# Performance work log

Hardware: AMD Instinct MI355X
Metric: run time of the kernel (lower is better)

## Reference

```python
import jax, jax.numpy as jnp
import numpy as np

B, D_IN, UNITS = 8192, 4096, 4096

def setup_inputs() -> dict:
    key = jax.random.key(0)
    k1, k2 = jax.random.split(key)
    x = jax.random.normal(k1, (B, D_IN), dtype=jnp.float32)
    kernel = jax.random.normal(k2, (D_IN, UNITS), dtype=jnp.float32) * 0.02  # glorot-ish scale
    bias = jnp.zeros((UNITS,), dtype=jnp.float32)
    return {"x": x, "kernel": kernel, "bias": bias}

def reference(x, kernel, bias):
    # BinaryDense: binarize weights via sign, then dense matmul + bias
    kernel_bin = jnp.sign(kernel)                     # [D_IN, UNITS], values in {-1,0,+1}
    out = jnp.matmul(x, kernel_bin) + bias            # [B, UNITS]
    return out
```

## Files before the change

### kernel.cpp

```cpp
#include <hip/hip_runtime.h>
#include <stdint.h>


typedef int int4v __attribute__((ext_vector_type(4)));

constexpr int M = 8192, N = 4096, K = 4096;
constexpr int BM = 256, BN = 256, BK = 128;
constexpr int NT = K / BK;
constexpr int NIT = NT / 2;

__device__ __forceinline__ void gload_lds16(const void* g, void* l) {
  __builtin_amdgcn_global_load_lds(
      (const __attribute__((address_space(1))) unsigned int*)g,
      (__attribute__((address_space(3))) unsigned int*)l, 16, 0, 0);
}

__global__ __launch_bounds__(256) void quant_x_kernel(const float* __restrict__ x,
                                                      signed char* __restrict__ xq,
                                                      float* __restrict__ rscale) {
  const int row = blockIdx.x;
  const int t = threadIdx.x;
  const float* xr = x + (size_t)row * K;
  float4 v[4];
  float mx = 0.f;
#pragma unroll
  for (int i = 0; i < 4; ++i) {
    v[i] = *(const float4*)(xr + t * 16 + i * 4);
    mx = fmaxf(mx, fmaxf(fmaxf(fabsf(v[i].x), fabsf(v[i].y)),
                         fmaxf(fabsf(v[i].z), fabsf(v[i].w))));
  }
#pragma unroll
  for (int off = 32; off >= 1; off >>= 1)
    mx = fmaxf(mx, __shfl_xor(mx, off, 64));
  __shared__ float smax[4];
  if ((t & 63) == 0) smax[t >> 6] = mx;
  __syncthreads();
  const float rm = fmaxf(fmaxf(smax[0], smax[1]), fmaxf(smax[2], smax[3]));
  const float s = (rm > 0.f) ? 127.f / rm : 0.f;
  if (t == 0) rscale[row] = (rm > 0.f) ? rm / 127.f : 0.f;
  uint32_t o[4];
#pragma unroll
  for (int i = 0; i < 4; ++i) {
    float f[4] = {v[i].x, v[i].y, v[i].z, v[i].w};
    uint32_t p = 0;
#pragma unroll
    for (int j = 0; j < 4; ++j) {
      int q = (int)rintf(f[j] * s);
      p |= ((uint32_t)(uint8_t)(signed char)q) << (8 * j);
    }
    o[i] = p;
  }
  *(int4v*)(xq + (size_t)row * K + t * 16) = (int4v){(int)o[0], (int)o[1], (int)o[2], (int)o[3]};
}

__global__ __launch_bounds__(256) void sign_t_kernel(const float* __restrict__ w,
                                                     signed char* __restrict__ wq) {
  __shared__ __align__(16) signed char tile[64 * 68];
  const int n0 = blockIdx.x * 64, k0 = blockIdx.y * 64;
  const int t = threadIdx.x;
#pragma unroll
  for (int i = 0; i < 4; ++i) {
    int kl = (t >> 4) + i * 16;
    int nl = (t & 15) * 4;
    float4 v = *(const float4*)(w + (size_t)(k0 + kl) * N + n0 + nl);
    uint32_t p = 0;
    p |= ((uint32_t)(uint8_t)(signed char)((v.x > 0.f) - (v.x < 0.f)));
    p |= ((uint32_t)(uint8_t)(signed char)((v.y > 0.f) - (v.y < 0.f))) << 8;
    p |= ((uint32_t)(uint8_t)(signed char)((v.z > 0.f) - (v.z < 0.f))) << 16;
    p |= ((uint32_t)(uint8_t)(signed char)((v.w > 0.f) - (v.w < 0.f))) << 24;
    *(uint32_t*)(tile + kl * 68 + nl) = p;
  }
  __syncthreads();
  const int nl = t >> 2;
  const int kc = (t & 3) * 16;
  uint32_t o[4] = {0, 0, 0, 0};
#pragma unroll
  for (int j = 0; j < 16; ++j)
    o[j >> 2] |= ((uint32_t)(uint8_t)tile[(kc + j) * 68 + nl]) << (8 * (j & 3));
  *(int4v*)(wq + (size_t)(n0 + nl) * K + k0 + kc) =
      (int4v){(int)o[0], (int)o[1], (int)o[2], (int)o[3]};
}


#define PHASE(BUF, MIH, NIH, LOADB, ...)                                         \
  {                                                                              \
    asm volatile("s_waitcnt vmcnt(6)" ::: "memory");                             \
    int4v a_[4][2];                                                              \
    _Pragma("unroll") for (int mi_ = 0; mi_ < 4; ++mi_) {                        \
      _Pragma("unroll") for (int kk_ = 0; kk_ < 2; ++kk_) {                      \
        const int row_ = wm * 128 + ((MIH)*4 + mi_) * 16 + l16;                  \
        const int c_ = kk_ * 4 + quad;                                           \
        a_[mi_][kk_] = *(const int4v*)(smem + (BUF)*65536 + row_ * 128 +         \
                                       ((c_ ^ (row_ & 7)) * 16));                \
      }                                                                          \
    }                                                                            \
    if (LOADB) {                                                                 \
      _Pragma("unroll") for (int nj_ = 0; nj_ < 2; ++nj_) {                      \
        _Pragma("unroll") for (int kk_ = 0; kk_ < 2; ++kk_) {                    \
          const int row_ = wn * 64 + ((NIH)*2 + nj_) * 16 + l16;                 \
          const int c_ = kk_ * 4 + quad;                                         \
          breg[nj_][kk_] = *(const int4v*)(smem + (BUF)*65536 + 32768 +          \
                                           row_ * 128 + ((c_ ^ (row_ & 7)) * 16)); \
        }                                                                        \
      }                                                                          \
    }                                                                            \
    __VA_ARGS__;                                                                 \
    __builtin_amdgcn_s_barrier();                                                \
    asm volatile("s_waitcnt lgkmcnt(0)" ::: "memory");                           \
    __builtin_amdgcn_s_setprio(1);                                               \
    _Pragma("unroll") for (int mi_ = 0; mi_ < 4; ++mi_) {                        \
      _Pragma("unroll") for (int nj_ = 0; nj_ < 2; ++nj_) {                      \
        _Pragma("unroll") for (int kk_ = 0; kk_ < 2; ++kk_) {                    \
          acc[(MIH)*4 + mi_][(NIH)*2 + nj_] =                                    \
              __builtin_amdgcn_mfma_i32_16x16x64_i8(                             \
                  a_[mi_][kk_], breg[nj_][kk_],                                  \
                  acc[(MIH)*4 + mi_][(NIH)*2 + nj_], 0, 0, 0);                   \
        }                                                                        \
      }                                                                          \
    }                                                                            \
    __builtin_amdgcn_s_setprio(0);                                               \
    __builtin_amdgcn_s_barrier();                                                \
  }

__global__ __launch_bounds__(512, 2) void gemm_bin_kernel(
    const signed char* __restrict__ Xq,
    const signed char* __restrict__ Wq,
    const float* __restrict__ rscale,
    const float* __restrict__ bias,
    float* __restrict__ out) {
  __shared__ __align__(16) signed char smem[131072];

  const int tid = threadIdx.x;
  const int w = tid >> 6;
  const int lane = tid & 63;
  const int wm = w >> 2;
  const int wn = w & 3;
  const int quad = lane >> 4;
  const int l16 = lane & 15;
  const size_t m0 = (size_t)blockIdx.y * BM;
  const size_t n0 = (size_t)blockIdx.x * BN;

  int4v acc[8][4];
#pragma unroll
  for (int i = 0; i < 8; ++i)
#pragma unroll
    for (int j = 0; j < 4; ++j) acc[i][j] = (int4v){0, 0, 0, 0};
  int4v breg[2][2];

  auto stageA = [&](int buf, int half, int tile) {
    signed char* lb = smem + buf * 65536;
#pragma unroll
    for (int it = 0; it < 2; ++it) {
      int pos = it * 512 + tid;
      int rr = pos >> 3, s = pos & 7;
      int row = half * 64 + (rr & 63) + (rr >> 6) * 128;
      int qg = s ^ (row & 7);
      gload_lds16(Xq + (m0 + row) * (size_t)K + (size_t)tile * BK + qg * 16,
                  lb + row * 128 + s * 16);
    }
  };
  auto stageB = [&](int buf, int half, int tile) {
    signed char* lb = smem + buf * 65536 + 32768;
#pragma unroll
    for (int it = 0; it < 2; ++it) {
      int pos = it * 512 + tid;
      int rr = pos >> 3, s = pos & 7;
      int row = half * 32 + (rr & 31) + (rr >> 5) * 64;
      int qg = s ^ (row & 7);
      gload_lds16(Wq + (n0 + row) * (size_t)K + (size_t)tile * BK + qg * 16,
                  lb + row * 128 + s * 16);
    }
  };

  stageB(0, 0, 0);
  stageA(0, 0, 0);
  stageA(0, 1, 0);
  stageB(0, 1, 0);
  stageB(1, 0, 1);
  stageA(1, 0, 1);
  asm volatile("s_waitcnt vmcnt(6)" ::: "memory");
  __builtin_amdgcn_s_barrier();

#pragma unroll 1
  for (int i = 0; i < NIT; ++i) {
    const int t1 = 2 * i + 1, t2 = 2 * i + 2, t3 = 2 * i + 3;
    const bool more = (i + 1 < NIT);
    PHASE(0, 0, 0, true,  { stageA(1, 1, t1); })
    PHASE(0, 1, 0, false, { stageB(1, 1, t1); })
    PHASE(0, 0, 1, true,  { if (more) stageB(0, 0, t2); })
    PHASE(0, 1, 1, false, { if (more) stageA(0, 0, t2); })
    PHASE(1, 0, 0, true,  { if (more) stageA(0, 1, t2); })
    PHASE(1, 1, 0, false, { if (more) stageB(0, 1, t2); })
    PHASE(1, 0, 1, true,  { if (more) stageB(1, 0, t3); })
    PHASE(1, 1, 1, false, { if (more) stageA(1, 0, t3); })
  }

#pragma unroll
  for (int mi = 0; mi < 8; ++mi) {
    const size_t rbase = m0 + wm * 128 + mi * 16 + quad * 4;
    float sc[4];
#pragma unroll
    for (int r = 0; r < 4; ++r) sc[r] = rscale[rbase + r];
#pragma unroll
    for (int ni = 0; ni < 4; ++ni) {
      const size_t col = n0 + wn * 64 + ni * 16 + l16;
      const float bv = bias[col];
#pragma unroll
      for (int r = 0; r < 4; ++r)
        out[(rbase + r) * N + col] = (float)acc[mi][ni][r] * sc[r] + bv;
    }
  }
}

extern "C" void kernel_launch(void* const* d_in, const int* in_sizes, int n_in,
                              void* d_out, int out_size, void* d_ws, size_t ws_size,
                              hipStream_t stream) {
  const float* x = (const float*)d_in[0];
  const float* kern = (const float*)d_in[1];
  const float* bias = (const float*)d_in[2];
  float* out = (float*)d_out;

  signed char* Xq = (signed char*)d_ws;
  signed char* Wq = Xq + (size_t)M * K;
  float* rscale = (float*)(Wq + (size_t)N * K);

  quant_x_kernel<<<M, 256, 0, stream>>>(x, Xq, rscale);
  sign_t_kernel<<<dim3(N / 64, K / 64), dim3(256), 0, stream>>>(kern, Wq);
  gemm_bin_kernel<<<dim3(N / BN, M / BM), 512, 0, stream>>>(Xq, Wq, rscale, bias, out);
}
```

Before: 394.6 us.

## Merge prep kernels and restructure GEMM pipeline to prefetch LDS fragments ahead of MFMA

Merges the x-quantization and weight sign-transpose kernels into one launch, removing one kernel launch and the serialization between them. The int8 GEMM main loop is reworked so each phase first issues the MFMAs on fragments already held in registers. It then reads the next phase's A/B fragments from LDS and issues the next global-to-LDS stage, with one barrier per phase instead of two. The tile staging order is reshuffled to match, and vmcnt is loosened to 4. This aims to overlap LDS reads with MFMA work, but adds register pressure from holding full A fragments and risks subtle LDS buffer hazards if the staging order is wrong.

```diff
diff --git a/kernel.cpp b/kernel.cpp
--- a/kernel.cpp
+++ b/kernel.cpp
@@ -15,111 +15,115 @@
       (__attribute__((address_space(3))) unsigned int*)l, 16, 0, 0);
 }
 
-__global__ __launch_bounds__(256) void quant_x_kernel(const float* __restrict__ x,
-                                                      signed char* __restrict__ xq,
-                                                      float* __restrict__ rscale) {
-  const int row = blockIdx.x;
+__global__ __launch_bounds__(256) void prep_kernel(const float* __restrict__ x,
+                                                   signed char* __restrict__ xq,
+                                                   float* __restrict__ rscale,
+                                                   const float* __restrict__ w,
+                                                   signed char* __restrict__ wq) {
   const int t = threadIdx.x;
-  const float* xr = x + (size_t)row * K;
-  float4 v[4];
-  float mx = 0.f;
-#pragma unroll
-  for (int i = 0; i < 4; ++i) {
-    v[i] = *(const float4*)(xr + t * 16 + i * 4);
-    mx = fmaxf(mx, fmaxf(fmaxf(fabsf(v[i].x), fabsf(v[i].y)),
-                         fmaxf(fabsf(v[i].z), fabsf(v[i].w))));
-  }
-#pragma unroll
-  for (int off = 32; off >= 1; off >>= 1)
-    mx = fmaxf(mx, __shfl_xor(mx, off, 64));
-  __shared__ float smax[4];
-  if ((t & 63) == 0) smax[t >> 6] = mx;
-  __syncthreads();
-  const float rm = fmaxf(fmaxf(smax[0], smax[1]), fmaxf(smax[2], smax[3]));
-  const float s = (rm > 0.f) ? 127.f / rm : 0.f;
-  if (t == 0) rscale[row] = (rm > 0.f) ? rm / 127.f : 0.f;
-  uint32_t o[4];
-#pragma unroll
-  for (int i = 0; i < 4; ++i) {
-    float f[4] = {v[i].x, v[i].y, v[i].z, v[i].w};
-    uint32_t p = 0;
-#pragma unroll
-    for (int j = 0; j < 4; ++j) {
-      int q = (int)rintf(f[j] * s);
-      p |= ((uint32_t)(uint8_t)(signed char)q) << (8 * j);
-    }
-    o[i] = p;
-  }
-  *(int4v*)(xq + (size_t)row * K + t * 16) = (int4v){(int)o[0], (int)o[1], (int)o[2], (int)o[3]};
-}
-
-__global__ __launch_bounds__(256) void sign_t_kernel(const float* __restrict__ w,
-                                                     signed char* __restrict__ wq) {
-  __shared__ __align__(16) signed char tile[64 * 68];
-  const int n0 = blockIdx.x * 64, k0 = blockIdx.y * 64;
-  const int t = threadIdx.x;
-#pragma unroll
-  for (int i = 0; i < 4; ++i) {
-    int kl = (t >> 4) + i * 16;
-    int nl = (t & 15) * 4;
-    float4 v = *(const float4*)(w + (size_t)(k0 + kl) * N + n0 + nl);
-    uint32_t p = 0;
-    p |= ((uint32_t)(uint8_t)(signed char)((v.x > 0.f) - (v.x < 0.f)));
-    p |= ((uint32_t)(uint8_t)(signed char)((v.y > 0.f) - (v.y < 0.f))) << 8;
-    p |= ((uint32_t)(uint8_t)(signed char)((v.z > 0.f) - (v.z < 0.f))) << 16;
-    p |= ((uint32_t)(uint8_t)(signed char)((v.w > 0.f) - (v.w < 0.f))) << 24;
-    *(uint32_t*)(tile + kl * 68 + nl) = p;
-  }
-  __syncthreads();
-  const int nl = t >> 2;
-  const int kc = (t & 3) * 16;
-  uint32_t o[4] = {0, 0, 0, 0};
-#pragma unroll
-  for (int j = 0; j < 16; ++j)
-    o[j >> 2] |= ((uint32_t)(uint8_t)tile[(kc + j) * 68 + nl]) << (8 * (j & 3));
-  *(int4v*)(wq + (size_t)(n0 + nl) * K + k0 + kc) =
-      (int4v){(int)o[0], (int)o[1], (int)o[2], (int)o[3]};
-}
-
-
-#define PHASE(BUF, MIH, NIH, LOADB, ...)                                         \
-  {                                                                              \
-    asm volatile("s_waitcnt vmcnt(6)" ::: "memory");                             \
-    int4v a_[4][2];                                                              \
-    _Pragma("unroll") for (int mi_ = 0; mi_ < 4; ++mi_) {                        \
-      _Pragma("unroll") for (int kk_ = 0; kk_ < 2; ++kk_) {                      \
-        const int row_ = wm * 128 + ((MIH)*4 + mi_) * 16 + l16;                  \
-        const int c_ = kk_ * 4 + quad;                                           \
-        a_[mi_][kk_] = *(const int4v*)(smem + (BUF)*65536 + row_ * 128 +         \
-                                       ((c_ ^ (row_ & 7)) * 16));                \
-      }                                                                          \
-    }                                                                            \
-    if (LOADB) {                                                                 \
-      _Pragma("unroll") for (int nj_ = 0; nj_ < 2; ++nj_) {                      \
-        _Pragma("unroll") for (int kk_ = 0; kk_ < 2; ++kk_) {                    \
-          const int row_ = wn * 64 + ((NIH)*2 + nj_) * 16 + l16;                 \
-          const int c_ = kk_ * 4 + quad;                                         \
-          breg[nj_][kk_] = *(const int4v*)(smem + (BUF)*65536 + 32768 +          \
-                                           row_ * 128 + ((c_ ^ (row_ & 7)) * 16)); \
-        }                                                                        \
-      }                                                                          \
-    }                                                                            \
-    __VA_ARGS__;                                                                 \
-    __builtin_amdgcn_s_barrier();                                                \
-    asm volatile("s_waitcnt lgkmcnt(0)" ::: "memory");                           \
-    __builtin_amdgcn_s_setprio(1);                                               \
-    _Pragma("unroll") for (int mi_ = 0; mi_ < 4; ++mi_) {                        \
-      _Pragma("unroll") for (int nj_ = 0; nj_ < 2; ++nj_) {                      \
-        _Pragma("unroll") for (int kk_ = 0; kk_ < 2; ++kk_) {                    \
-          acc[(MIH)*4 + mi_][(NIH)*2 + nj_] =                                    \
-              __builtin_amdgcn_mfma_i32_16x16x64_i8(                             \
-                  a_[mi_][kk_], breg[nj_][kk_],                                  \
-                  acc[(MIH)*4 + mi_][(NIH)*2 + nj_], 0, 0, 0);                   \
-        }                                                                        \
-      }                                                                          \
-    }                                                                            \
-    __builtin_amdgcn_s_setprio(0);                                               \
-    __builtin_amdgcn_s_barrier();                                                \
+  if (blockIdx.x < M) {
+    const int row = blockIdx.x;
+    const float* xr = x + (size_t)row * K;
+    float4 v[4];
+    float mx = 0.f;
+#pragma unroll
+    for (int i = 0; i < 4; ++i) {
+      v[i] = *(const float4*)(xr + t * 16 + i * 4);
+      mx = fmaxf(mx, fmaxf(fmaxf(fabsf(v[i].x), fabsf(v[i].y)),
+                           fmaxf(fabsf(v[i].z), fabsf(v[i].w))));
+    }
+#pragma unroll
+    for (int off = 32; off >= 1; off >>= 1)
+      mx = fmaxf(mx, __shfl_xor(mx, off, 64));
+    __shared__ float smax[4];
+    if ((t & 63) == 0) smax[t >> 6] = mx;
+    __syncthreads();
+    const float rm = fmaxf(fmaxf(smax[0], smax[1]), fmaxf(smax[2], smax[3]));
+    const float s = (rm > 0.f) ? 127.f / rm : 0.f;
+    if (t == 0) rscale[row] = (rm > 0.f) ? rm / 127.f : 0.f;
+    uint32_t o[4];
+#pragma unroll
+    for (int i = 0; i < 4; ++i) {
+      float f[4] = {v[i].x, v[i].y, v[i].z, v[i].w};
+      uint32_t p = 0;
+#pragma unroll
+      for (int j = 0; j < 4; ++j) {
+        int q = (int)rintf(f[j] * s);
+        p |= ((uint32_t)(uint8_t)(signed char)q) << (8 * j);
+      }
+      o[i] = p;
+    }
+    *(int4v*)(xq + (size_t)row * K + t * 16) =
+        (int4v){(int)o[0], (int)o[1], (int)o[2], (int)o[3]};
+  } else {
+    __shared__ __align__(16) signed char tile[64 * 68];
+    const int idx = blockIdx.x - M;
+    const int n0 = (idx & 63) * 64, k0 = (idx >> 6) * 64;
+#pragma unroll
+    for (int i = 0; i < 4; ++i) {
+      int kl = (t >> 4) + i * 16;
+      int nl = (t & 15) * 4;
+      float4 v = *(const float4*)(w + (size_t)(k0 + kl) * N + n0 + nl);
+      uint32_t p = 0;
+      p |= ((uint32_t)(uint8_t)(signed char)((v.x > 0.f) - (v.x < 0.f)));
+      p |= ((uint32_t)(uint8_t)(signed char)((v.y > 0.f) - (v.y < 0.f))) << 8;
+      p |= ((uint32_t)(uint8_t)(signed char)((v.z > 0.f) - (v.z < 0.f))) << 16;
+      p |= ((uint32_t)(uint8_t)(signed char)((v.w > 0.f) - (v.w < 0.f))) << 24;
+      *(uint32_t*)(tile + kl * 68 + nl) = p;
+    }
+    __syncthreads();
+    const int nl = t >> 2;
+    const int kc = (t & 3) * 16;
+    uint32_t o[4] = {0, 0, 0, 0};
+#pragma unroll
+    for (int j = 0; j < 16; ++j)
+      o[j >> 2] |= ((uint32_t)(uint8_t)tile[(kc + j) * 68 + nl]) << (8 * (j & 3));
+    *(int4v*)(wq + (size_t)(n0 + nl) * K + k0 + kc) =
+        (int4v){(int)o[0], (int)o[1], (int)o[2], (int)o[3]};
+  }
+}
+
+
+#define RD_A(BUF, HALF)                                                       \
+  {                                                                           \
+    _Pragma("unroll") for (int mi_ = 0; mi_ < 4; ++mi_) {                     \
+      _Pragma("unroll") for (int kk_ = 0; kk_ < 2; ++kk_) {                   \
+        const int r_ = wm * 128 + (HALF)*64 + mi_ * 16 + l16;                 \
+        a[mi_][kk_] = *(const int4v*)(smem + (BUF)*65536 + r_ * 128 +         \
+                                      (((kk_ * 4 + quad) ^ (r_ & 7)) * 16));  \
+      }                                                                       \
+    }                                                                         \
+  }
+
+#define RD_B(BUF, HALF)                                                       \
+  {                                                                           \
+    _Pragma("unroll") for (int nj_ = 0; nj_ < 2; ++nj_) {                     \
+      _Pragma("unroll") for (int kk_ = 0; kk_ < 2; ++kk_) {                   \
+        const int r_ = wn * 64 + (HALF)*32 + nj_ * 16 + l16;                  \
+        b[nj_][kk_] = *(const int4v*)(smem + (BUF)*65536 + 32768 + r_ * 128 + \
+                                      (((kk_ * 4 + quad) ^ (r_ & 7)) * 16));  \
+      }                                                                       \
+    }                                                                         \
+  }
+
+#define PH(MIH, NIH, RDBLK, STBLK)                                            \
+  {                                                                           \
+    __builtin_amdgcn_s_setprio(1);                                            \
+    _Pragma("unroll") for (int kk_ = 0; kk_ < 2; ++kk_) {                     \
+      _Pragma("unroll") for (int mi_ = 0; mi_ < 4; ++mi_) {                   \
+        _Pragma("unroll") for (int nj_ = 0; nj_ < 2; ++nj_) {                 \
+          acc[(MIH)*4 + mi_][(NIH)*2 + nj_] =                                 \
+              __builtin_amdgcn_mfma_i32_16x16x64_i8(                          \
+                  a[mi_][kk_], b[nj_][kk_],                                   \
+                  acc[(MIH)*4 + mi_][(NIH)*2 + nj_], 0, 0, 0);                \
+        }                                                                     \
+      }                                                                       \
+    }                                                                         \
+    __builtin_amdgcn_s_setprio(0);                                            \
+    RDBLK;                                                                    \
+    STBLK;                                                                    \
+    asm volatile("s_waitcnt vmcnt(4)" ::: "memory");                          \
+    __builtin_amdgcn_s_barrier();                                             \
   }
 
 __global__ __launch_bounds__(512, 2) void gemm_bin_kernel(
@@ -145,7 +149,8 @@
   for (int i = 0; i < 8; ++i)
 #pragma unroll
     for (int j = 0; j < 4; ++j) acc[i][j] = (int4v){0, 0, 0, 0};
-  int4v breg[2][2];
+  int4v a[4][2];
+  int4v b[2][2];
 
   auto stageA = [&](int buf, int half, int tile) {
     signed char* lb = smem + buf * 65536;
@@ -177,22 +182,25 @@
   stageA(0, 1, 0);
   stageB(0, 1, 0);
   stageB(1, 0, 1);
-  stageA(1, 0, 1);
+  stageA(1, 1, 1);
+  stageB(1, 1, 1);
   asm volatile("s_waitcnt vmcnt(6)" ::: "memory");
   __builtin_amdgcn_s_barrier();
+  RD_A(0, 0);
+  RD_B(0, 0);
 
 #pragma unroll 1
   for (int i = 0; i < NIT; ++i) {
     const int t1 = 2 * i + 1, t2 = 2 * i + 2, t3 = 2 * i + 3;
     const bool more = (i + 1 < NIT);
-    PHASE(0, 0, 0, true,  { stageA(1, 1, t1); })
-    PHASE(0, 1, 0, false, { stageB(1, 1, t1); })
-    PHASE(0, 0, 1, true,  { if (more) stageB(0, 0, t2); })
-    PHASE(0, 1, 1, false, { if (more) stageA(0, 0, t2); })
-    PHASE(1, 0, 0, true,  { if (more) stageA(0, 1, t2); })
-    PHASE(1, 1, 0, false, { if (more) stageB(0, 1, t2); })
-    PHASE(1, 0, 1, true,  { if (more) stageB(1, 0, t3); })
-    PHASE(1, 1, 1, false, { if (more) stageA(1, 0, t3); })
+    PH(0, 0, { RD_A(0, 1); }, { stageA(1, 0, t1); })
+    PH(1, 0, { RD_B(0, 1); }, { if (more) stageB(0, 0, t2); })
+    PH(1, 1, { RD_A(0, 0); }, { if (more) stageA(0, 1, t2); })
+    PH(0, 1, { RD_A(1, 0); RD_B(1, 0); }, { if (more) stageB(0, 1, t2); })
+    PH(0, 0, { RD_A(1, 1); }, { if (more) stageA(0, 0, t2); })
+    PH(1, 0, { RD_B(1, 1); }, { if (more) stageB(1, 0, t3); })
+    PH(1, 1, { RD_A(1, 0); }, { if (more) stageA(1, 1, t3); })
+    PH(0, 1, { RD_A(0, 0); RD_B(0, 0); }, { if (more) stageB(1, 1, t3); })
   }
 
 #pragma unroll
@@ -224,7 +232,6 @@
   signed char* Wq = Xq + (size_t)M * K;
   float* rscale = (float*)(Wq + (size_t)N * K);
 
-  quant_x_kernel<<<M, 256, 0, stream>>>(x, Xq, rscale);
-  sign_t_kernel<<<dim3(N / 64, K / 64), dim3(256), 0, stream>>>(kern, Wq);
+  prep_kernel<<<M + (N / 64) * (K / 64), 256, 0, stream>>>(x, Xq, rscale, kern, Wq);
   gemm_bin_kernel<<<dim3(N / BN, M / BM), 512, 0, stream>>>(Xq, Wq, rscale, bias, out);
 }
```

Measured after the change: 378.3 us. -4.1%, faster.
